# Performance work log

Hardware: AMD Instinct MI355X
Metric: run time of the kernel (lower is better)

Reference implementation:

```python
import jax, jax.numpy as jnp
import numpy as np

HIDDEN = 128
STATE = 64
ACTION = 16
D_IO = STATE + ACTION  # 80
BATCH = 4096
SEQ_LEN = 512


def setup_inputs() -> dict:
    key = jax.random.key(0)
    ks = jax.random.split(key, 7)
    s = 1.0 / np.sqrt(HIDDEN)
    return {
        "quantized_hn": jax.random.normal(ks[0], (BATCH, HIDDEN), jnp.float32),
        "W_ih": jax.random.uniform(ks[1], (4 * HIDDEN, D_IO), jnp.float32, -s, s),
        "W_hh": jax.random.uniform(ks[2], (4 * HIDDEN, HIDDEN), jnp.float32, -s, s),
        "b_ih": jax.random.uniform(ks[3], (4 * HIDDEN,), jnp.float32, -s, s),
        "b_hh": jax.random.uniform(ks[4], (4 * HIDDEN,), jnp.float32, -s, s),
        "W_fc": jax.random.uniform(ks[5], (D_IO, HIDDEN), jnp.float32, -s, s),
        "b_fc": jax.random.uniform(ks[6], (D_IO,), jnp.float32, -s, s),
        "seq_len": SEQ_LEN,
    }


def reference(quantized_hn, W_ih, W_hh, b_ih, b_hh, W_fc, b_fc, seq_len):
    B, H = quantized_hn.shape
    D = W_fc.shape[0]

    def step(carry, _):
        h, c, x = carry  # h,c: (B,H); x: (B,D)
        # PyTorch LSTM gate order: i, f, g, o
        gates = x @ W_ih.T + b_ih + h @ W_hh.T + b_hh  # (B, 4H)
        i, f, g, o = jnp.split(gates, 4, axis=-1)
        c_new = jax.nn.sigmoid(f) * c + jax.nn.sigmoid(i) * jnp.tanh(g)
        h_new = jax.nn.sigmoid(o) * jnp.tanh(c_new)
        y = h_new @ W_fc.T + b_fc  # (B, D) -> fed back as next input
        return (h_new, c_new, y), y

    h0 = quantized_hn
    c0 = jnp.zeros((B, H), quantized_hn.dtype)
    x0 = jnp.zeros((B, D), quantized_hn.dtype)
    _, ys = jax.lax.scan(step, (h0, c0, x0), None, length=seq_len)
    return jnp.transpose(ys, (1, 0, 2))  # (B, seq_len, D)
```

## Files before the change

### kernel.cpp

```cpp
#include <hip/hip_runtime.h>

typedef __bf16 bf16_t;
typedef __bf16 bf16x4 __attribute__((ext_vector_type(4)));
typedef __bf16 bf16x8 __attribute__((ext_vector_type(8)));
typedef float  f32x4  __attribute__((ext_vector_type(4)));
typedef int    i32x4  __attribute__((ext_vector_type(4)));

#define HID    128
#define DIO    80
#define G4     512
#define TSTEP  512
#define BB     16
#define NBATCH 4096
#define NBLK   (NBATCH / BB)
#define HSTR   136

__device__ __align__(16) bf16_t g_weff_frags[128 * 512];
__device__ __align__(16) bf16_t g_whh_frags[128 * 512];
__device__ __align__(16) bf16_t g_wfc_frags[20 * 512];
__device__ float g_weff[G4 * HID];
__device__ float g_beff[G4];
__device__ float g_b1[G4];

__global__ void k_weff(const float* __restrict__ W_ih, const float* __restrict__ W_hh,
                       const float* __restrict__ b_ih, const float* __restrict__ b_hh,
                       const float* __restrict__ W_fc, const float* __restrict__ b_fc) {
  int gid = blockIdx.x * blockDim.x + threadIdx.x;
  int g = gid >> 7, k = gid & 127;
  float acc = W_hh[g * HID + k];
#pragma unroll 8
  for (int d = 0; d < DIO; ++d)
    acc = fmaf(W_ih[g * DIO + d], W_fc[d * HID + k], acc);
  g_weff[g * HID + k] = acc;
  if (k == 0) {
    float bb = b_ih[g] + b_hh[g];
    g_b1[g] = bb;
    float be = bb;
    for (int d = 0; d < DIO; ++d) be = fmaf(W_ih[g * DIO + d], b_fc[d], be);
    g_beff[g] = be;
  }
}

__global__ void k_frag(const float* __restrict__ W_hh, const float* __restrict__ W_fc) {
  int tile = blockIdx.x;
  int lane = threadIdx.x;
  int c = lane & 15, q = lane >> 4;
  if (tile < 128) {
    int gtile = tile >> 2, kt = tile & 3;
    int n = gtile * 16 + c;
#pragma unroll
    for (int j = 0; j < 8; ++j)
      g_weff_frags[tile * 512 + lane * 8 + j] = (bf16_t)g_weff[n * HID + kt * 32 + q * 8 + j];
  } else if (tile < 256) {
    int t2 = tile - 128;
    int gtile = t2 >> 2, kt = t2 & 3;
    int n = gtile * 16 + c;
#pragma unroll
    for (int j = 0; j < 8; ++j)
      g_whh_frags[t2 * 512 + lane * 8 + j] = (bf16_t)W_hh[n * HID + kt * 32 + q * 8 + j];
  } else {
    int t2 = tile - 256;
    int yt = t2 >> 2, kt = t2 & 3;
    int n = yt * 16 + c;
#pragma unroll
    for (int j = 0; j < 8; ++j)
      g_wfc_frags[t2 * 512 + lane * 8 + j] = (bf16_t)W_fc[n * HID + kt * 32 + q * 8 + j];
  }
}

__device__ __forceinline__ float fsigm(float x) {
  return __builtin_amdgcn_rcpf(1.0f + __builtin_amdgcn_exp2f(x * -1.4426950408889634f));
}
__device__ __forceinline__ float ftanh(float x) {
  return 1.0f - 2.0f * __builtin_amdgcn_rcpf(1.0f + __builtin_amdgcn_exp2f(x * 2.8853900817779268f));
}

__global__ __launch_bounds__(512, 2) void k_lstm(const float* __restrict__ h0,
                                                 const float* __restrict__ b_fc,
                                                 float* __restrict__ out) {
  __shared__ __align__(16) bf16_t hbuf[2][BB * HSTR];
  const int tid = threadIdx.x;
  const int lane = tid & 63;
  const int w = tid >> 6;
  const int c = lane & 15, q = lane >> 4;
  const int b0 = blockIdx.x * BB;

  for (int i = tid; i < BB * HID; i += 512) {
    int r = i >> 7, k = i & 127;
    hbuf[0][r * HSTR + k] = (bf16_t)h0[(long)(b0 + r) * HID + k];
  }

  i32x4 Wy[4];
  f32x4 ybias;
  if (w < 5) {
#pragma unroll
    for (int kt = 0; kt < 4; ++kt) {
      Wy[kt] = *(const i32x4*)&g_wfc_frags[(w * 4 + kt) * 512 + lane * 8];
      asm volatile("" : "+v"(Wy[kt]));
    }
#pragma unroll
    for (int r = 0; r < 4; ++r) ybias[r] = b_fc[w * 16 + q * 4 + r];
    asm volatile("" : "+v"(ybias));
  }

  i32x4 Wg[4][4];
  f32x4 bias[4];
  auto load_wg = [&](const bf16_t* frags, const float* bsrc) {
#pragma unroll
    for (int G = 0; G < 4; ++G) {
      int gtile = G * 8 + w;
#pragma unroll
      for (int r = 0; r < 4; ++r) bias[G][r] = bsrc[gtile * 16 + q * 4 + r];
#pragma unroll
      for (int kt = 0; kt < 4; ++kt)
        Wg[G][kt] = *(const i32x4*)&frags[(gtile * 4 + kt) * 512 + lane * 8];
    }
  };
  auto pin_wg = [&]() {
#pragma unroll
    for (int G = 0; G < 4; ++G) {
      asm volatile("" : "+v"(bias[G]));
#pragma unroll
      for (int kt = 0; kt < 4; ++kt) asm volatile("" : "+v"(Wg[G][kt]));
    }
  };

  f32x4 cst = (f32x4){0, 0, 0, 0};
  bf16x8 hf[4];

  __syncthreads();
#pragma unroll
  for (int kt = 0; kt < 4; ++kt)
    hf[kt] = *(const bf16x8*)&hbuf[0][c * HSTR + kt * 32 + q * 8];

  float* outp = out + (long)(b0 + c) * TSTEP * DIO + w * 16 + q * 4;

  auto step = [&](int t) {
    f32x4 acc[4];
#pragma unroll
    for (int G = 0; G < 4; ++G) acc[G] = bias[G];
#pragma unroll
    for (int kt = 0; kt < 4; ++kt)
#pragma unroll
      for (int G = 0; G < 4; ++G)
        acc[G] = __builtin_amdgcn_mfma_f32_16x16x32_bf16(
            __builtin_bit_cast(bf16x8, Wg[G][kt]), hf[kt], acc[G], 0, 0, 0);

    const int buf = t & 1;
    bf16x4 hv;
#pragma unroll
    for (int r = 0; r < 4; ++r) {
      float iv = fsigm(acc[0][r]);
      float fv = fsigm(acc[1][r]);
      float gv = ftanh(acc[2][r]);
      float ov = fsigm(acc[3][r]);
      float cn = fv * cst[r] + iv * gv;
      cst[r] = cn;
      hv[r] = (bf16_t)(ov * ftanh(cn));
    }
    *(bf16x4*)&hbuf[buf][c * HSTR + w * 16 + q * 4] = hv;
    __syncthreads();
#pragma unroll
    for (int kt = 0; kt < 4; ++kt)
      hf[kt] = *(const bf16x8*)&hbuf[buf][c * HSTR + kt * 32 + q * 8];

    if (w < 5) {
      f32x4 ya = ybias;
#pragma unroll
      for (int kt = 0; kt < 4; ++kt)
        ya = __builtin_amdgcn_mfma_f32_16x16x32_bf16(
            __builtin_bit_cast(bf16x8, Wy[kt]), hf[kt], ya, 0, 0, 0);
      *(f32x4*)&outp[(long)(t - 1) * DIO] = ya;
    }
  };

  load_wg(g_whh_frags, g_b1);
  step(1);
  load_wg(g_weff_frags, g_beff);
  pin_wg();
#pragma unroll 1
  for (int t = 2; t <= TSTEP; ++t) step(t);
}

extern "C" void kernel_launch(void* const* d_in, const int* in_sizes, int n_in,
                              void* d_out, int out_size, void* d_ws, size_t ws_size,
                              hipStream_t stream) {
  const float* h0   = (const float*)d_in[0];
  const float* W_ih = (const float*)d_in[1];
  const float* W_hh = (const float*)d_in[2];
  const float* b_ih = (const float*)d_in[3];
  const float* b_hh = (const float*)d_in[4];
  const float* W_fc = (const float*)d_in[5];
  const float* b_fc = (const float*)d_in[6];
  float* out = (float*)d_out;

  k_weff<<<256, 256, 0, stream>>>(W_ih, W_hh, b_ih, b_hh, W_fc, b_fc);
  k_frag<<<276, 64, 0, stream>>>(W_hh, W_fc);
  k_lstm<<<NBLK, 512, 0, stream>>>(h0, b_fc, out);
}
```

Before: 1.004 ms.

## Halve batch per block, move output weights and biases to LDS, fuse activations

Reduces the batch rows per block from 16 to 8, padding the 16-wide MFMA tile with zero rows, and raises launch bounds to 4 blocks per CU. This doubles the block count and spreads the sequential recurrence over more CUs. The output-projection weights and all biases move from registers into shared memory to lower VGPR pressure. The gate math is rewritten with fewer reciprocals by merging sigmoid(i)*tanh(g) and sigmoid(o)*tanh(c). The output projection is reordered to run before the elementwise step so it overlaps, at the cost of half-wasted MFMA work and extra LDS reads every step.

```diff
diff --git a/kernel.cpp b/kernel.cpp
--- a/kernel.cpp
+++ b/kernel.cpp
@@ -10,7 +10,7 @@
 #define DIO    80
 #define G4     512
 #define TSTEP  512
-#define BB     16
+#define BB     8
 #define NBATCH 4096
 #define NBLK   (NBATCH / BB)
 #define HSTR   136
@@ -68,61 +68,43 @@
   }
 }
 
-__device__ __forceinline__ float fsigm(float x) {
-  return __builtin_amdgcn_rcpf(1.0f + __builtin_amdgcn_exp2f(x * -1.4426950408889634f));
-}
-__device__ __forceinline__ float ftanh(float x) {
-  return 1.0f - 2.0f * __builtin_amdgcn_rcpf(1.0f + __builtin_amdgcn_exp2f(x * 2.8853900817779268f));
-}
-
-__global__ __launch_bounds__(512, 2) void k_lstm(const float* __restrict__ h0,
+#define LOG2E 1.4426950408889634f
+
+__global__ __launch_bounds__(512, 4) void k_lstm(const float* __restrict__ h0,
                                                  const float* __restrict__ b_fc,
                                                  float* __restrict__ out) {
-  __shared__ __align__(16) bf16_t hbuf[2][BB * HSTR];
+  __shared__ __align__(16) bf16_t hbuf[2][16 * HSTR];
+  __shared__ __align__(16) bf16_t wyl[20 * 512];
+  __shared__ __align__(16) float beffl[G4];
+  __shared__ __align__(16) float b1l[G4];
+  __shared__ __align__(16) float bfcl[DIO];
   const int tid = threadIdx.x;
   const int lane = tid & 63;
   const int w = tid >> 6;
   const int c = lane & 15, q = lane >> 4;
   const int b0 = blockIdx.x * BB;
 
+  for (int i = tid; i < 2 * 8 * HID; i += 512) {
+    int buf = i >> 10, idx = i & 1023;
+    hbuf[buf][(8 + (idx >> 7)) * HSTR + (idx & 127)] = (bf16_t)0.0f;
+  }
   for (int i = tid; i < BB * HID; i += 512) {
     int r = i >> 7, k = i & 127;
     hbuf[0][r * HSTR + k] = (bf16_t)h0[(long)(b0 + r) * HID + k];
   }
-
-  i32x4 Wy[4];
-  f32x4 ybias;
-  if (w < 5) {
-#pragma unroll
-    for (int kt = 0; kt < 4; ++kt) {
-      Wy[kt] = *(const i32x4*)&g_wfc_frags[(w * 4 + kt) * 512 + lane * 8];
-      asm volatile("" : "+v"(Wy[kt]));
-    }
-#pragma unroll
-    for (int r = 0; r < 4; ++r) ybias[r] = b_fc[w * 16 + q * 4 + r];
-    asm volatile("" : "+v"(ybias));
-  }
+  for (int i = tid; i < 20 * 512 / 2; i += 512)
+    ((int*)wyl)[i] = ((const int*)g_wfc_frags)[i];
+  beffl[tid < G4 ? tid : 0] = g_beff[tid < G4 ? tid : 0];
+  b1l[tid < G4 ? tid : 0] = g_b1[tid < G4 ? tid : 0];
+  if (tid < DIO) bfcl[tid] = b_fc[tid];
 
   i32x4 Wg[4][4];
-  f32x4 bias[4];
-  auto load_wg = [&](const bf16_t* frags, const float* bsrc) {
-#pragma unroll
-    for (int G = 0; G < 4; ++G) {
-      int gtile = G * 8 + w;
-#pragma unroll
-      for (int r = 0; r < 4; ++r) bias[G][r] = bsrc[gtile * 16 + q * 4 + r];
+  auto load_wg = [&](const bf16_t* frags) {
+#pragma unroll
+    for (int G = 0; G < 4; ++G)
 #pragma unroll
       for (int kt = 0; kt < 4; ++kt)
-        Wg[G][kt] = *(const i32x4*)&frags[(gtile * 4 + kt) * 512 + lane * 8];
-    }
-  };
-  auto pin_wg = [&]() {
-#pragma unroll
-    for (int G = 0; G < 4; ++G) {
-      asm volatile("" : "+v"(bias[G]));
-#pragma unroll
-      for (int kt = 0; kt < 4; ++kt) asm volatile("" : "+v"(Wg[G][kt]));
-    }
+        Wg[G][kt] = *(const i32x4*)&frags[((G * 8 + w) * 4 + kt) * 512 + lane * 8];
   };
 
   f32x4 cst = (f32x4){0, 0, 0, 0};
@@ -135,51 +117,82 @@
 
   float* outp = out + (long)(b0 + c) * TSTEP * DIO + w * 16 + q * 4;
 
-  auto step = [&](int t) {
+  auto elemwise = [&](f32x4 acc[4], int buf) {
+    bf16x4 hv;
+#pragma unroll
+    for (int r = 0; r < 4; ++r) {
+      float a = __builtin_amdgcn_exp2f(acc[0][r] * -LOG2E);
+      float b = __builtin_amdgcn_exp2f(acc[2][r] * (2.f * LOG2E));
+      float e = __builtin_amdgcn_exp2f(acc[1][r] * -LOG2E);
+      float u = __builtin_amdgcn_exp2f(acc[3][r] * -LOG2E);
+      float sf = __builtin_amdgcn_rcpf(1.0f + e);
+      float itg = (b - 1.0f) * __builtin_amdgcn_rcpf(fmaf(a, b, a + b) + 1.0f);
+      float cn = fmaf(sf, cst[r], itg);
+      cst[r] = cn;
+      float v = __builtin_amdgcn_exp2f(cn * (2.f * LOG2E));
+      hv[r] = (bf16_t)((v - 1.0f) * __builtin_amdgcn_rcpf(fmaf(u, v, u + v) + 1.0f));
+    }
+    if (c < 8) *(bf16x4*)&hbuf[buf][c * HSTR + w * 16 + q * 4] = hv;
+  };
+
+  load_wg(g_whh_frags);
+  {
     f32x4 acc[4];
 #pragma unroll
-    for (int G = 0; G < 4; ++G) acc[G] = bias[G];
+    for (int G = 0; G < 4; ++G)
+      acc[G] = *(const f32x4*)&b1l[(G * 8 + w) * 16 + q * 4];
 #pragma unroll
     for (int kt = 0; kt < 4; ++kt)
 #pragma unroll
       for (int G = 0; G < 4; ++G)
         acc[G] = __builtin_amdgcn_mfma_f32_16x16x32_bf16(
             __builtin_bit_cast(bf16x8, Wg[G][kt]), hf[kt], acc[G], 0, 0, 0);
-
-    const int buf = t & 1;
-    bf16x4 hv;
-#pragma unroll
-    for (int r = 0; r < 4; ++r) {
-      float iv = fsigm(acc[0][r]);
-      float fv = fsigm(acc[1][r]);
-      float gv = ftanh(acc[2][r]);
-      float ov = fsigm(acc[3][r]);
-      float cn = fv * cst[r] + iv * gv;
-      cst[r] = cn;
-      hv[r] = (bf16_t)(ov * ftanh(cn));
-    }
-    *(bf16x4*)&hbuf[buf][c * HSTR + w * 16 + q * 4] = hv;
+    elemwise(acc, 1);
     __syncthreads();
 #pragma unroll
     for (int kt = 0; kt < 4; ++kt)
-      hf[kt] = *(const bf16x8*)&hbuf[buf][c * HSTR + kt * 32 + q * 8];
+      hf[kt] = *(const bf16x8*)&hbuf[1][c * HSTR + kt * 32 + q * 8];
+  }
+
+  load_wg(g_weff_frags);
+#pragma unroll 1
+  for (int t = 2; t <= TSTEP; ++t) {
+    f32x4 acc[4];
+#pragma unroll
+    for (int G = 0; G < 4; ++G)
+      acc[G] = *(const f32x4*)&beffl[(G * 8 + w) * 16 + q * 4];
+#pragma unroll
+    for (int kt = 0; kt < 4; ++kt)
+#pragma unroll
+      for (int G = 0; G < 4; ++G)
+        acc[G] = __builtin_amdgcn_mfma_f32_16x16x32_bf16(
+            __builtin_bit_cast(bf16x8, Wg[G][kt]), hf[kt], acc[G], 0, 0, 0);
 
     if (w < 5) {
-      f32x4 ya = ybias;
+      f32x4 ya = *(const f32x4*)&bfcl[w * 16 + q * 4];
 #pragma unroll
       for (int kt = 0; kt < 4; ++kt)
         ya = __builtin_amdgcn_mfma_f32_16x16x32_bf16(
-            __builtin_bit_cast(bf16x8, Wy[kt]), hf[kt], ya, 0, 0, 0);
-      *(f32x4*)&outp[(long)(t - 1) * DIO] = ya;
+            *(const bf16x8*)&wyl[(w * 4 + kt) * 512 + lane * 8], hf[kt], ya, 0, 0, 0);
+      if (c < 8) *(f32x4*)&outp[(long)(t - 2) * DIO] = ya;
     }
-  };
-
-  load_wg(g_whh_frags, g_b1);
-  step(1);
-  load_wg(g_weff_frags, g_beff);
-  pin_wg();
-#pragma unroll 1
-  for (int t = 2; t <= TSTEP; ++t) step(t);
+
+    const int buf = t & 1;
+    elemwise(acc, buf);
+    __syncthreads();
+#pragma unroll
+    for (int kt = 0; kt < 4; ++kt)
+      hf[kt] = *(const bf16x8*)&hbuf[buf][c * HSTR + kt * 32 + q * 8];
+  }
+
+  if (w < 5) {
+    f32x4 ya = *(const f32x4*)&bfcl[w * 16 + q * 4];
+#pragma unroll
+    for (int kt = 0; kt < 4; ++kt)
+      ya = __builtin_amdgcn_mfma_f32_16x16x32_bf16(
+          *(const bf16x8*)&wyl[(w * 4 + kt) * 512 + lane * 8], hf[kt], ya, 0, 0, 0);
+    if (c < 8) *(f32x4*)&outp[(long)(TSTEP - 1) * DIO] = ya;
+  }
 }
 
 extern "C" void kernel_launch(void* const* d_in, const int* in_sizes, int n_in,
```

Result: slower. 1.336 ms (+33.1%).
